# Kernel tuning notes

Hardware: AMD Instinct MI355X
Metric: run time of the kernel (lower is better)

The kernel has to match this reference:

```python
import jax, jax.numpy as jnp
import numpy as np

P_BINS = 5
T_BINS = 16
B_BINS = P_BINS * T_BINS  # 80
IN_CH = 16
OUT_CH = 32
N_VERTS = 30000   # mesh vertices (cols of conn)
N_PATCH = 30000   # patches (rows of conn / B)
K_NNZ = 3         # nnz per sparse row (interpolation support)


def setup_inputs() -> dict:
    key = jax.random.key(0)
    k1, k2, k3, k4 = jax.random.split(key, 4)
    x = jax.random.normal(k1, (N_VERTS, IN_CH), dtype=jnp.float32)
    conn_idx = jax.random.randint(k2, (N_PATCH * B_BINS, K_NNZ), 0, N_VERTS, dtype=jnp.int32)
    conn_val = jax.random.uniform(k3, (N_PATCH * B_BINS, K_NNZ), dtype=jnp.float32)
    weights = jax.random.normal(k4, (B_BINS, IN_CH, OUT_CH), dtype=jnp.float32)
    return {"x": x, "conn_idx": conn_idx, "conn_val": conn_val, "weights": weights}


def _rotated_weights(weights):
    # layer_weights[j, :, :, i] = weights[(j + p*i) % B]  -> reshape (B*inp, out*t)
    j = jnp.arange(B_BINS)[:, None]
    i = jnp.arange(T_BINS)[None, :]
    idx = (j + P_BINS * i) % B_BINS                       # (B, t)
    lw = weights[idx]                                     # (B, t, inp, out)
    lw = jnp.transpose(lw, (0, 2, 3, 1))                  # (B, inp, out, t)
    return lw.reshape(B_BINS * IN_CH, OUT_CH * T_BINS)


def reference(x, conn_idx, conn_val, weights):
    # sparse.mm(conn, x): gather K vertex features per bin row and weight-sum
    gathered = jnp.einsum('rk,rkc->rc', conn_val, x[conn_idx])  # (N*B, inp)
    h = gathered.reshape(-1, B_BINS * IN_CH)                    # (N, B*inp)
    lw = _rotated_weights(weights)                              # (B*inp, out*t)
    y = h @ lw                                                  # (N, out*t)
    y = y.reshape(-1, OUT_CH, T_BINS)
    return jnp.max(y, axis=-1)                                  # (N, out)
```

## Files before the change

kernel.cpp:

```cpp
#include <hip/hip_runtime.h>
#include <hip/hip_bf16.h>
#include <stdint.h>

#define NP 30000
#define BBINS 80
#define INCH 16
#define OUTCH 32
#define KDIM 1280
#define NDIM 512
#define KSTEPS 40
#define NROWS (NP * BBINS)
#define RPT 4
#define RSTRIDE (NROWS / RPT)

typedef __bf16 bf16x8 __attribute__((ext_vector_type(8)));
typedef __bf16 bf16x4 __attribute__((ext_vector_type(4)));
typedef float f32x4 __attribute__((ext_vector_type(4)));

__device__ __forceinline__ void async_ld16(const void* g, void* l) {
    __builtin_amdgcn_global_load_lds(
        (const __attribute__((address_space(1))) unsigned int*)g,
        (__attribute__((address_space(3))) unsigned int*)l,
        16, 0, 0);
}

__global__ void prep_weights(const float* __restrict__ w, __bf16* __restrict__ pw) {
    int gid = blockIdx.x * 256 + threadIdx.x;
    int e  = gid & 7;
    int qs = (gid >> 3) & 3;
    int n  = (gid >> 5) & 511;
    int kc = gid >> 14;
    int kp = kc * 32 + ((qs ^ ((n >> 1) & 3)) << 3) + e;
    int b = kp >> 4, c = kp & 15;
    int o = n >> 4,  t = n & 15;
    int bid = (b + 5 * t) % BBINS;
    pw[gid] = (__bf16)w[(bid * INCH + c) * OUTCH + o];
}

__global__ __launch_bounds__(256) void gather_h(
    const float* __restrict__ x,
    const int*   __restrict__ cidx,
    const float* __restrict__ cval,
    __bf16* __restrict__ h) {
    const int gid = blockIdx.x * 256 + threadIdx.x;
    const int rb = gid >> 2;
    const int q  = gid & 3;

    int   i0[RPT], i1[RPT], i2[RPT];
    float v0[RPT], v1[RPT], v2[RPT];
#pragma unroll
    for (int k = 0; k < RPT; ++k) {
        const int r3 = (rb + k * RSTRIDE) * 3;
        i0[k] = cidx[r3 + 0]; i1[k] = cidx[r3 + 1]; i2[k] = cidx[r3 + 2];
        v0[k] = cval[r3 + 0]; v1[k] = cval[r3 + 1]; v2[k] = cval[r3 + 2];
    }
    float4 a[RPT], b[RPT], c[RPT];
#pragma unroll
    for (int k = 0; k < RPT; ++k) {
        a[k] = *(const float4*)(x + (size_t)i0[k] * 16 + q * 4);
        b[k] = *(const float4*)(x + (size_t)i1[k] * 16 + q * 4);
        c[k] = *(const float4*)(x + (size_t)i2[k] * 16 + q * 4);
    }
#pragma unroll
    for (int k = 0; k < RPT; ++k) {
        bf16x4 hv;
        hv[0] = (__bf16)(v0[k] * a[k].x + v1[k] * b[k].x + v2[k] * c[k].x);
        hv[1] = (__bf16)(v0[k] * a[k].y + v1[k] * b[k].y + v2[k] * c[k].y);
        hv[2] = (__bf16)(v0[k] * a[k].z + v1[k] * b[k].z + v2[k] * c[k].z);
        hv[3] = (__bf16)(v0[k] * a[k].w + v1[k] * b[k].w + v2[k] * c[k].w);
        *(bf16x4*)((char*)h + (size_t)(rb + k * RSTRIDE) * 32 + q * 8) = hv;
    }
}

__global__ __launch_bounds__(256, 2) void gemm_max(
    const __bf16* __restrict__ h,
    const __bf16* __restrict__ pw,
    float* __restrict__ out) {

    __shared__ __align__(16) __bf16 Alds[2][128 * 32];
    __shared__ __align__(16) __bf16 Blds[2][256 * 32];

    const int bid = blockIdx.x;
    const int m    = (bid >> 4) * 8 + (bid & 7);
    const int ncol = (bid >> 3) & 1;
    if (m >= 235) return;
    const int mbase = m * 128;

    const int tid  = threadIdx.x;
    const int lane = tid & 63;
    const int wave = tid >> 6;
    const int wave_mrow = wave >> 1;
    const int wave_ncol = wave & 1;

    int a_off[4], b_off[8];
    {
        const int ml = lane & 15, q = lane >> 4;
        const int f = (ml >> 1) & 3;
#pragma unroll
        for (int i = 0; i < 4; ++i)
            a_off[i] = (wave_mrow * 64 + i * 16 + ml) * 64 + ((q ^ f) << 4);
#pragma unroll
        for (int j = 0; j < 8; ++j) {
            int nl = wave_ncol * 128 + j * 16 + ml;
            b_off[j] = nl * 64 + ((q ^ f) << 4);
        }
    }

    f32x4 acc[4][8];
#pragma unroll
    for (int i = 0; i < 4; ++i)
#pragma unroll
        for (int j = 0; j < 8; ++j)
            acc[i][j] = (f32x4){0.f, 0.f, 0.f, 0.f};

    const char* hB  = (const char*)h;
    const char* pwB = (const char*)pw + ncol * 16384 + tid * 16;
    int rg0 = mbase + (tid >> 2);
    int rg1 = rg0 + 64;
    if (rg0 > NP - 1) rg0 = NP - 1;
    if (rg1 > NP - 1) rg1 = NP - 1;
    const int swz = ((tid & 3) ^ ((tid >> 3) & 3)) * 16;
    const char* aSrc0 = hB + (size_t)rg0 * 2560 + swz;
    const char* aSrc1 = hB + (size_t)rg1 * 2560 + swz;
    char* aDstB = (char*)Alds + tid * 16;
    char* bDstB = (char*)Blds + tid * 16;

#define STAGE(kc_, buf_)                                                     \
    do {                                                                     \
        const char* bs_ = pwB + (kc_) * 32768;                               \
        char* bD_ = bDstB + (buf_) * 16384;                                  \
        char* aD_ = aDstB + (buf_) * 8192;                                   \
        async_ld16(bs_ + 0 * 4096, bD_ + 0 * 4096);                          \
        async_ld16(bs_ + 1 * 4096, bD_ + 1 * 4096);                          \
        async_ld16(bs_ + 2 * 4096, bD_ + 2 * 4096);                          \
        async_ld16(bs_ + 3 * 4096, bD_ + 3 * 4096);                          \
        async_ld16(aSrc0 + (kc_) * 64, aD_);                                 \
        async_ld16(aSrc1 + (kc_) * 64, aD_ + 4096);                          \
    } while (0)

    STAGE(0, 0);
    asm volatile("s_waitcnt vmcnt(0)" ::: "memory");
    __builtin_amdgcn_s_barrier();

    for (int kc = 0; kc < KSTEPS; ++kc) {
        const int cur = kc & 1;
        if (kc + 1 < KSTEPS)
            STAGE(kc + 1, cur ^ 1);

        const char* A = (const char*)Alds + cur * 8192;
        const char* B = (const char*)Blds + cur * 16384;
        bf16x8 af[4], bfr[8];
#pragma unroll
        for (int i = 0; i < 4; ++i)
            af[i] = *(const bf16x8*)(A + a_off[i]);
#pragma unroll
        for (int j = 0; j < 8; ++j)
            bfr[j] = *(const bf16x8*)(B + b_off[j]);
#pragma unroll
        for (int i = 0; i < 4; ++i)
#pragma unroll
            for (int j = 0; j < 8; ++j)
                acc[i][j] = __builtin_amdgcn_mfma_f32_16x16x32_bf16(
                    af[i], bfr[j], acc[i][j], 0, 0, 0);

        asm volatile("s_waitcnt vmcnt(0)" ::: "memory");
        __builtin_amdgcn_s_barrier();
    }
#undef STAGE

    const int rgrp = lane >> 4;
    const int tl   = lane & 15;
#pragma unroll
    for (int i = 0; i < 4; ++i) {
#pragma unroll
        for (int j = 0; j < 8; ++j) {
            float v0 = acc[i][j][0], v1 = acc[i][j][1];
            float v2 = acc[i][j][2], v3 = acc[i][j][3];
#pragma unroll
            for (int off = 1; off < 16; off <<= 1) {
                v0 = fmaxf(v0, __shfl_xor(v0, off));
                v1 = fmaxf(v1, __shfl_xor(v1, off));
                v2 = fmaxf(v2, __shfl_xor(v2, off));
                v3 = fmaxf(v3, __shfl_xor(v3, off));
            }
            if (tl == 0) {
                const int o  = ncol * 16 + wave_ncol * 8 + j;
                const int pr = mbase + wave_mrow * 64 + i * 16 + rgrp * 4;
                if (pr + 0 < NP) out[(pr + 0) * 32 + o] = v0;
                if (pr + 1 < NP) out[(pr + 1) * 32 + o] = v1;
                if (pr + 2 < NP) out[(pr + 2) * 32 + o] = v2;
                if (pr + 3 < NP) out[(pr + 3) * 32 + o] = v3;
            }
        }
    }
}

extern "C" void kernel_launch(void* const* d_in, const int* in_sizes, int n_in,
                              void* d_out, int out_size, void* d_ws, size_t ws_size,
                              hipStream_t stream) {
    const float* x    = (const float*)d_in[0];
    const int*   cidx = (const int*)d_in[1];
    const float* cval = (const float*)d_in[2];
    const float* w    = (const float*)d_in[3];
    float* out = (float*)d_out;

    __bf16* pw = (__bf16*)d_ws;
    __bf16* h  = (__bf16*)((char*)d_ws + (2 << 20));

    hipLaunchKernelGGL(prep_weights, dim3(2560), dim3(256), 0, stream, w, pw);
    hipLaunchKernelGGL(gather_h, dim3(NROWS / 256), dim3(256), 0, stream,
                       x, cidx, cval, h);
    hipLaunchKernelGGL(gemm_max, dim3(480), dim3(256), 0, stream,
                       h, (const __bf16*)pw, out);
}
```

Before: 202.1 us.

## Load A fragments directly from global and single-buffer B in LDS

```diff
diff --git a/kernel.cpp b/kernel.cpp
--- a/kernel.cpp
+++ b/kernel.cpp
@@ -77,8 +77,7 @@
     const __bf16* __restrict__ pw,
     float* __restrict__ out) {
 
-    __shared__ __align__(16) __bf16 Alds[2][128 * 32];
-    __shared__ __align__(16) __bf16 Blds[2][256 * 32];
+    __shared__ __align__(16) __bf16 Blds[256 * 32];
 
     const int bid = blockIdx.x;
     const int m    = (bid >> 4) * 8 + (bid & 7);
@@ -92,18 +91,21 @@
     const int wave_mrow = wave >> 1;
     const int wave_ncol = wave & 1;
 
-    int a_off[4], b_off[8];
-    {
-        const int ml = lane & 15, q = lane >> 4;
-        const int f = (ml >> 1) & 3;
-#pragma unroll
-        for (int i = 0; i < 4; ++i)
-            a_off[i] = (wave_mrow * 64 + i * 16 + ml) * 64 + ((q ^ f) << 4);
-#pragma unroll
-        for (int j = 0; j < 8; ++j) {
-            int nl = wave_ncol * 128 + j * 16 + ml;
-            b_off[j] = nl * 64 + ((q ^ f) << 4);
-        }
+    const int ml = lane & 15, q = lane >> 4;
+    const int f = (ml >> 1) & 3;
+    int b_off[8];
+#pragma unroll
+    for (int j = 0; j < 8; ++j) {
+        int nl = wave_ncol * 128 + j * 16 + ml;
+        b_off[j] = nl * 64 + ((q ^ f) << 4);
+    }
+
+    const char* aPtr[4];
+#pragma unroll
+    for (int i = 0; i < 4; ++i) {
+        int r = mbase + wave_mrow * 64 + i * 16 + ml;
+        if (r > NP - 1) r = NP - 1;
+        aPtr[i] = (const char*)h + (size_t)r * 2560 + q * 16;
     }
 
     f32x4 acc[4][8];
@@ -113,49 +115,30 @@
         for (int j = 0; j < 8; ++j)
             acc[i][j] = (f32x4){0.f, 0.f, 0.f, 0.f};
 
-    const char* hB  = (const char*)h;
     const char* pwB = (const char*)pw + ncol * 16384 + tid * 16;
-    int rg0 = mbase + (tid >> 2);
-    int rg1 = rg0 + 64;
-    if (rg0 > NP - 1) rg0 = NP - 1;
-    if (rg1 > NP - 1) rg1 = NP - 1;
-    const int swz = ((tid & 3) ^ ((tid >> 3) & 3)) * 16;
-    const char* aSrc0 = hB + (size_t)rg0 * 2560 + swz;
-    const char* aSrc1 = hB + (size_t)rg1 * 2560 + swz;
-    char* aDstB = (char*)Alds + tid * 16;
-    char* bDstB = (char*)Blds + tid * 16;
-
-#define STAGE(kc_, buf_)                                                     \
+    char* bDst = (char*)Blds + tid * 16;
+
+#define STAGE_B(kc_)                                                         \
     do {                                                                     \
         const char* bs_ = pwB + (kc_) * 32768;                               \
-        char* bD_ = bDstB + (buf_) * 16384;                                  \
-        char* aD_ = aDstB + (buf_) * 8192;                                   \
-        async_ld16(bs_ + 0 * 4096, bD_ + 0 * 4096);                          \
-        async_ld16(bs_ + 1 * 4096, bD_ + 1 * 4096);                          \
-        async_ld16(bs_ + 2 * 4096, bD_ + 2 * 4096);                          \
-        async_ld16(bs_ + 3 * 4096, bD_ + 3 * 4096);                          \
-        async_ld16(aSrc0 + (kc_) * 64, aD_);                                 \
-        async_ld16(aSrc1 + (kc_) * 64, aD_ + 4096);                          \
+        async_ld16(bs_ + 0 * 4096, bDst + 0 * 4096);                         \
+        async_ld16(bs_ + 1 * 4096, bDst + 1 * 4096);                         \
+        async_ld16(bs_ + 2 * 4096, bDst + 2 * 4096);                         \
+        async_ld16(bs_ + 3 * 4096, bDst + 3 * 4096);                         \
     } while (0)
 
-    STAGE(0, 0);
-    asm volatile("s_waitcnt vmcnt(0)" ::: "memory");
-    __builtin_amdgcn_s_barrier();
+    bf16x8 af[4];
+    STAGE_B(0);
+#pragma unroll
+    for (int i = 0; i < 4; ++i)
+        af[i] = *(const bf16x8*)(aPtr[i]);
+    __syncthreads();
 
     for (int kc = 0; kc < KSTEPS; ++kc) {
-        const int cur = kc & 1;
-        if (kc + 1 < KSTEPS)
-            STAGE(kc + 1, cur ^ 1);
-
-        const char* A = (const char*)Alds + cur * 8192;
-        const char* B = (const char*)Blds + cur * 16384;
-        bf16x8 af[4], bfr[8];
-#pragma unroll
-        for (int i = 0; i < 4; ++i)
-            af[i] = *(const bf16x8*)(A + a_off[i]);
+        bf16x8 bfr[8];
 #pragma unroll
         for (int j = 0; j < 8; ++j)
-            bfr[j] = *(const bf16x8*)(B + b_off[j]);
+            bfr[j] = *(const bf16x8*)((const char*)Blds + b_off[j]);
 #pragma unroll
         for (int i = 0; i < 4; ++i)
 #pragma unroll
@@ -163,10 +146,16 @@
                 acc[i][j] = __builtin_amdgcn_mfma_f32_16x16x32_bf16(
                     af[i], bfr[j], acc[i][j], 0, 0, 0);
 
-        asm volatile("s_waitcnt vmcnt(0)" ::: "memory");
-        __builtin_amdgcn_s_barrier();
-    }
-#undef STAGE
+        if (kc + 1 < KSTEPS) {
+            __syncthreads();
+            STAGE_B(kc + 1);
+#pragma unroll
+            for (int i = 0; i < 4; ++i)
+                af[i] = *(const bf16x8*)(aPtr[i] + (kc + 1) * 64);
+            __syncthreads();
+        }
+    }
+#undef STAGE_B
 
     const int rgrp = lane >> 4;
     const int tl   = lane & 15;
```

Result: slower. 210.1 us (+4.0%).
